# Kernel optimization log

Hardware: AMD Instinct MI355X
Metric: run time of the kernel (lower is better)

## Reference

```python
import jax, jax.numpy as jnp
import numpy as np

N = 50000          # nodes
E = 800000         # edges (before self loops)
D_IN = 128         # input_dim
HID = 64           # hidden_dim (per head)
HEADS = 2
DM = HID * HEADS   # 128, post-concat dim
OUT = 32           # out_channels
G = 64             # graphs in batch
EPS = 1e-5
SLOPE = 0.2        # GATConv negative_slope default


def setup_inputs() -> dict:
    key = jax.random.key(0)
    ks = jax.random.split(key, 24)
    s = 0.1
    return {
        "x": jax.random.normal(ks[0], (N, D_IN), jnp.float32),
        "edge_index": jax.random.randint(ks[1], (2, E), 0, N, jnp.int32),
        "batch": jnp.sort(jax.random.randint(ks[2], (N,), 0, G, jnp.int32)),
        # GAT layer 1
        "W1": jax.random.normal(ks[3], (D_IN, DM), jnp.float32) * s,
        "att_src1": jax.random.normal(ks[4], (HEADS, HID), jnp.float32) * s,
        "att_dst1": jax.random.normal(ks[5], (HEADS, HID), jnp.float32) * s,
        "b1": jnp.zeros((DM,), jnp.float32),
        "ln1_g": jnp.ones((DM,), jnp.float32),
        "ln1_b": jnp.zeros((DM,), jnp.float32),
        # skip connection
        "Wskip": jax.random.normal(ks[6], (D_IN, DM), jnp.float32) * s,
        "bskip": jnp.zeros((DM,), jnp.float32),
        # GAT layer 2
        "W2": jax.random.normal(ks[7], (DM, DM), jnp.float32) * s,
        "att_src2": jax.random.normal(ks[8], (HEADS, HID), jnp.float32) * s,
        "att_dst2": jax.random.normal(ks[9], (HEADS, HID), jnp.float32) * s,
        "b2": jnp.zeros((DM,), jnp.float32),
        "ln2_g": jnp.ones((DM,), jnp.float32),
        "ln2_b": jnp.zeros((DM,), jnp.float32),
        # head
        "Wfc": jax.random.normal(ks[10], (DM, OUT), jnp.float32) * s,
        "bfc": jnp.zeros((OUT,), jnp.float32),
        "bn_g": jnp.ones((OUT,), jnp.float32),
        "bn_b": jnp.zeros((OUT,), jnp.float32),
    }


def _layer_norm(x, g, b):
    m = x.mean(-1, keepdims=True)
    v = ((x - m) ** 2).mean(-1, keepdims=True)
    return (x - m) * jax.lax.rsqrt(v + EPS) * g + b


def _gat(h_in, W, att_src, att_dst, bias, src, dst):
    # PyG GATConv (concat=True): h = x W reshaped to [N,H,C]
    h = (h_in @ W).reshape(N, HEADS, HID)
    a_src = (h * att_src).sum(-1)   # [N,H]
    a_dst = (h * att_dst).sum(-1)   # [N,H]
    e = jax.nn.leaky_relu(a_src[src] + a_dst[dst], SLOPE)  # [E',H]
    # segment softmax over edges sharing target node
    e = e - jax.ops.segment_max(e, dst, num_segments=N)[dst]
    ee = jnp.exp(e)
    denom = jax.ops.segment_sum(ee, dst, num_segments=N)[dst]
    alpha = ee / denom
    msg = h[src] * alpha[:, :, None]               # [E',H,C]
    out = jax.ops.segment_sum(msg, dst, num_segments=N)  # [N,H,C]
    return out.reshape(N, DM) + bias


def reference(x, edge_index, batch, W1, att_src1, att_dst1, b1, ln1_g, ln1_b,
              Wskip, bskip, W2, att_src2, att_dst2, b2, ln2_g, ln2_b,
              Wfc, bfc, bn_g, bn_b):
    # add self loops (PyG GATConv default)
    loop = jnp.arange(N, dtype=edge_index.dtype)
    src = jnp.concatenate([edge_index[0], loop])
    dst = jnp.concatenate([edge_index[1], loop])

    x1 = _gat(x, W1, att_src1, att_dst1, b1, src, dst)
    x1 = jax.nn.elu(_layer_norm(x1, ln1_g, ln1_b))
    x1 = x1 + (x @ Wskip + bskip)          # dropout = identity (eval)

    x2 = _gat(x1, W2, att_src2, att_dst2, b2, src, dst)
    x2 = _layer_norm(x2 + x1, ln2_g, ln2_b)
    emb = jax.nn.elu(x2)

    # global mean pool per graph
    sums = jax.ops.segment_sum(emb, batch, num_segments=G)
    cnt = jax.ops.segment_sum(jnp.ones((N,), emb.dtype), batch, num_segments=G)
    graph_emb = sums / jnp.maximum(cnt, 1.0)[:, None]

    logits = graph_emb @ Wfc + bfc
    # BatchNorm1d (training-mode batch stats, biased var)
    m = logits.mean(0)
    v = ((logits - m) ** 2).mean(0)
    return (logits - m) * jax.lax.rsqrt(v + EPS) * bn_g + bn_b
```

## Files before the change

kernel.cpp:

```cpp
#include <hip/hip_runtime.h>

#define DM    128
#define NHEAD 2
#define HIDC  64
#define OUTC  32
#define NG    64
#define EPS   1e-5f
#define DCAP  64

typedef __attribute__((ext_vector_type(8))) short bf16x8;
typedef __attribute__((ext_vector_type(4))) float f32x4;

__device__ __forceinline__ unsigned short f2bf(float f) {
    union { float f; unsigned int u; } v; v.f = f;
    unsigned int r = v.u + 0x7fffu + ((v.u >> 16) & 1u);
    return (unsigned short)(r >> 16);
}
__device__ __forceinline__ float bflo(unsigned int u) {
    union { unsigned int u; float f; } v; v.u = u << 16; return v.f;
}
__device__ __forceinline__ float bfhi(unsigned int u) {
    union { unsigned int u; float f; } v; v.u = u & 0xffff0000u; return v.f;
}

__global__ void wprep_kernel(const float* __restrict__ W,
                             unsigned short* __restrict__ Wfrag)
{
    const int idx = blockIdx.x * blockDim.x + threadIdx.x;
    if (idx >= 8 * 4 * 64) return;
    const int nt   = idx >> 8;
    const int ks   = (idx >> 6) & 3;
    const int lane = idx & 63;
    const int c    = nt * 16 + (lane & 15);
    const int k0   = ks * 32 + (lane >> 4) * 8;
    bf16x8 f;
#pragma unroll
    for (int j = 0; j < 8; ++j)
        f[j] = (short)f2bf(W[(k0 + j) * DM + c]);
    ((bf16x8*)Wfrag)[idx] = f;
}

__global__ void xprep_kernel(const float* __restrict__ X,
                             unsigned short* __restrict__ Xb, int total)
{
    const int i = (blockIdx.x * blockDim.x + threadIdx.x) * 4;
    if (i >= total) return;
    const float4 v = *(const float4*)&X[i];
    ushort4 o;
    o.x = f2bf(v.x); o.y = f2bf(v.y); o.z = f2bf(v.z); o.w = f2bf(v.w);
    *(ushort4*)&Xb[i] = o;
}

__global__ __launch_bounds__(256) void mfma_gemm_kernel(
    const unsigned short* __restrict__ Xbf, int N,
    const unsigned short* __restrict__ Wfrag,
    const float* __restrict__ bias,
    const float* __restrict__ att_src,
    const float* __restrict__ att_dst,
    float* __restrict__ C,
    unsigned short* __restrict__ Cbf,
    float* __restrict__ a_src,
    float* __restrict__ a_dst)
{
    const int lane = threadIdx.x & 63;
    const int wave = threadIdx.x >> 6;
    const int col  = lane & 15;
    const int kgrp = lane >> 4;

    bf16x8 bfrag[8][4];
    {
        const bf16x8* wf = (const bf16x8*)Wfrag;
#pragma unroll
        for (int nt = 0; nt < 8; ++nt)
#pragma unroll
            for (int ks = 0; ks < 4; ++ks)
                bfrag[nt][ks] = wf[(nt * 4 + ks) * 64 + lane];
    }

    float bcol[8];
#pragma unroll
    for (int nt = 0; nt < 8; ++nt)
        bcol[nt] = bias ? bias[nt * 16 + col] : 0.f;

    float as_c[8], ad_c[8];
    if (att_src) {
#pragma unroll
        for (int nt = 0; nt < 8; ++nt) {
            as_c[nt] = att_src[nt * 16 + col];
            ad_c[nt] = att_dst[nt * 16 + col];
        }
    }

    const int ntiles = (N + 15) >> 4;
    for (int tile = blockIdx.x * 4 + wave; tile < ntiles; tile += gridDim.x * 4) {
        const int row0 = tile * 16;

        f32x4 acc[8];
#pragma unroll
        for (int nt = 0; nt < 8; ++nt) acc[nt] = (f32x4){0.f, 0.f, 0.f, 0.f};

        const int r = min(row0 + col, N - 1);
#pragma unroll
        for (int ks = 0; ks < 4; ++ks) {
            const int k0 = ks * 32 + kgrp * 8;
            const bf16x8 af = *(const bf16x8*)&Xbf[(size_t)r * DM + k0];
#pragma unroll
            for (int nt = 0; nt < 8; ++nt)
                acc[nt] = __builtin_amdgcn_mfma_f32_16x16x32_bf16(
                              af, bfrag[nt][ks], acc[nt], 0, 0, 0);
        }

        float dots[4][2], dotd[4][2];
        if (att_src) {
#pragma unroll
            for (int reg = 0; reg < 4; ++reg) {
                dots[reg][0] = dots[reg][1] = 0.f;
                dotd[reg][0] = dotd[reg][1] = 0.f;
            }
        }
#pragma unroll
        for (int reg = 0; reg < 4; ++reg) {
            const int row = row0 + kgrp * 4 + reg;
            const bool ok = row < N;
#pragma unroll
            for (int nt = 0; nt < 8; ++nt) {
                const float o = acc[nt][reg] + bcol[nt];
                if (ok) {
                    if (Cbf) Cbf[(size_t)row * DM + nt * 16 + col] = f2bf(o);
                    else     C  [(size_t)row * DM + nt * 16 + col] = o;
                }
                if (att_src) {
                    dots[reg][nt >> 2] += o * as_c[nt];
                    dotd[reg][nt >> 2] += o * ad_c[nt];
                }
            }
        }
        if (att_src) {
#pragma unroll
            for (int reg = 0; reg < 4; ++reg) {
#pragma unroll
                for (int h = 0; h < 2; ++h) {
                    float vs = dots[reg][h], vd = dotd[reg][h];
#pragma unroll
                    for (int off = 8; off; off >>= 1) {
                        vs += __shfl_xor(vs, off);
                        vd += __shfl_xor(vd, off);
                    }
                    const int row = row0 + kgrp * 4 + reg;
                    if (col == 0 && row < N) {
                        a_src[row * NHEAD + h] = vs;
                        a_dst[row * NHEAD + h] = vd;
                    }
                }
            }
        }
    }
}

__global__ void scatter_kernel(const int* __restrict__ ei, int E,
                               int* __restrict__ cursor,
                               unsigned short* __restrict__ col)
{
    int e = blockIdx.x * blockDim.x + threadIdx.x;
    if (e < E) {
        int d = ei[E + e];
        int k = atomicAdd(&cursor[d], 1);
        if (k < DCAP) col[d * DCAP + k] = (unsigned short)ei[e];
    }
}

__global__ __launch_bounds__(128) void gat_agg_ln_kernel(
    const int* __restrict__ deg,
    const unsigned short* __restrict__ col,
    const unsigned short* __restrict__ H,
    const float* __restrict__ a_src,
    const float* __restrict__ a_dst,
    const float* __restrict__ bias,
    const float* __restrict__ res,
    const float* __restrict__ lng,
    const float* __restrict__ lnb,
    const float* __restrict__ skip,
    float* __restrict__ out,
    unsigned short* __restrict__ obf,
    int N)
{
    const int wid  = threadIdx.x >> 6;
    const int d    = blockIdx.x * 2 + wid;
    if (d >= N) return;
    const int lane = threadIdx.x & 63;
    const int half = lane >> 5;
    const int c2   = lane * 2;

    const float ad_h = a_dst[d * NHEAD + half];

    float e0 = a_src[d * NHEAD + half] + ad_h;
    e0 = e0 > 0.f ? e0 : 0.2f * e0;
    const float wself = __expf(e0);
    float den = wself;
    float2 acc;
    {
        const unsigned int hu = *(const unsigned int*)&H[(size_t)d * DM + c2];
        acc.x = wself * bflo(hu);
        acc.y = wself * bfhi(hu);
    }

    const int dg = min(deg[d], DCAP);
    const int p0 = d * DCAP;
    for (int base = 0; base < dg; base += 32) {
        const int m = min(32, dg - base);
        const int el = lane & 31;

        float we = 0.f;
        int s = 0;
        if (el < m) {
            s = (int)col[p0 + base + el];
            float a = a_src[s * NHEAD + half] + ad_h;
            a = a > 0.f ? a : 0.2f * a;
            we = __expf(a);
        }
        float ws = we;
#pragma unroll
        for (int off = 1; off < 32; off <<= 1) ws += __shfl_xor(ws, off);
        den += ws;

        const int hsel = lane & 32;
        int e = 0;
        for (; e + 8 <= m; e += 8) {
            int   sv[8];
            float wv[8];
            unsigned int uv[8];
#pragma unroll
            for (int j = 0; j < 8; ++j) {
                sv[j] = __shfl(s, e + j);
                wv[j] = __shfl(we, hsel | (e + j));
            }
#pragma unroll
            for (int j = 0; j < 8; ++j)
                uv[j] = *(const unsigned int*)&H[(size_t)sv[j] * DM + c2];
#pragma unroll
            for (int j = 0; j < 8; ++j) {
                acc.x += wv[j] * bflo(uv[j]);
                acc.y += wv[j] * bfhi(uv[j]);
            }
        }
        for (; e < m; ++e) {
            const int sE = __shfl(s, e);
            const float wE = __shfl(we, hsel | e);
            const unsigned int uE = *(const unsigned int*)&H[(size_t)sE * DM + c2];
            acc.x += wE * bflo(uE);
            acc.y += wE * bfhi(uE);
        }
    }

    const size_t ibase = (size_t)d * DM + c2;
    const float2 bv = *(const float2*)&bias[c2];
    float vx = acc.x / den + bv.x;
    float vy = acc.y / den + bv.y;
    if (res) {
        const float2 r = *(const float2*)&res[ibase];
        vx += r.x; vy += r.y;
    }

    float sm = vx + vy;
#pragma unroll
    for (int off = 1; off < 64; off <<= 1) sm += __shfl_xor(sm, off);
    const float mean = sm * (1.f / DM);

    const float dx = vx - mean, dy = vy - mean;
    float s2 = dx * dx + dy * dy;
#pragma unroll
    for (int off = 1; off < 64; off <<= 1) s2 += __shfl_xor(s2, off);
    const float rstd = rsqrtf(s2 * (1.f / DM) + EPS);

    const float2 gv = *(const float2*)&lng[c2];
    const float2 bb = *(const float2*)&lnb[c2];
    float yx = dx * rstd * gv.x + bb.x;
    float yy = dy * rstd * gv.y + bb.y;
    yx = yx > 0.f ? yx : expm1f(yx);
    yy = yy > 0.f ? yy : expm1f(yy);
    if (skip) {
        const float2 sk = *(const float2*)&skip[ibase];
        yx += sk.x; yy += sk.y;
    }
    *(float2*)&out[ibase] = make_float2(yx, yy);
    if (obf) {
        const unsigned int pk = (unsigned int)f2bf(yx) |
                                ((unsigned int)f2bf(yy) << 16);
        *(unsigned int*)&obf[ibase] = pk;
    }
}

__global__ void pool_kernel(const float* __restrict__ emb,
                            const int* __restrict__ batch, int N,
                            float* __restrict__ sums,
                            float* __restrict__ cnt)
{
    const int t = threadIdx.x;
    const int chunk = (N + gridDim.x - 1) / gridDim.x;
    const int n0 = blockIdx.x * chunk;
    const int n1 = min(N, n0 + chunk);
    if (n0 >= n1) return;

    int cur = batch[n0];
    float acc = 0.f;
    int count = 0;
    for (int n = n0; n < n1; ++n) {
        int b = batch[n];
        if (b != cur) {
            atomicAdd(&sums[cur * DM + t], acc);
            if (t == 0) atomicAdd(&cnt[cur], (float)count);
            acc = 0.f; count = 0; cur = b;
        }
        acc += emb[n * DM + t];
        ++count;
    }
    atomicAdd(&sums[cur * DM + t], acc);
    if (t == 0) atomicAdd(&cnt[cur], (float)count);
}

__global__ void head_kernel(const float* __restrict__ sums,
                            const float* __restrict__ cnt,
                            const float* __restrict__ Wfc,
                            const float* __restrict__ bfc,
                            const float* __restrict__ bn_g,
                            const float* __restrict__ bn_b,
                            float* __restrict__ out)
{
    __shared__ float ge[NG * DM];
    __shared__ float lg[NG * OUTC];
    __shared__ float mu[OUTC], inv[OUTC];
    const int t = threadIdx.x;

    for (int i = t; i < NG * DM; i += blockDim.x) {
        int g = i >> 7;
        ge[i] = sums[i] / fmaxf(cnt[g], 1.0f);
    }
    __syncthreads();

    for (int i = t; i < NG * OUTC; i += blockDim.x) {
        int g = i >> 5, o = i & (OUTC - 1);
        float acc = bfc[o];
#pragma unroll
        for (int k = 0; k < DM; ++k) acc += ge[g * DM + k] * Wfc[k * OUTC + o];
        lg[i] = acc;
    }
    __syncthreads();

    if (t < OUTC) {
        float s = 0.f;
        for (int g = 0; g < NG; ++g) s += lg[g * OUTC + t];
        float m = s * (1.f / NG);
        float v = 0.f;
        for (int g = 0; g < NG; ++g) { float d = lg[g * OUTC + t] - m; v += d * d; }
        v *= (1.f / NG);
        mu[t] = m;
        inv[t] = rsqrtf(v + EPS) * bn_g[t];
    }
    __syncthreads();

    for (int i = t; i < NG * OUTC; i += blockDim.x) {
        int o = i & (OUTC - 1);
        out[i] = (lg[i] - mu[o]) * inv[o] + bn_b[o];
    }
}

extern "C" void kernel_launch(void* const* d_in, const int* in_sizes, int n_in,
                              void* d_out, int out_size, void* d_ws, size_t ws_size,
                              hipStream_t stream)
{
    const float* x     = (const float*)d_in[0];
    const int*   ei    = (const int*)  d_in[1];
    const int*   batch = (const int*)  d_in[2];
    const float* W1    = (const float*)d_in[3];
    const float* as1   = (const float*)d_in[4];
    const float* ad1   = (const float*)d_in[5];
    const float* b1    = (const float*)d_in[6];
    const float* ln1g  = (const float*)d_in[7];
    const float* ln1b  = (const float*)d_in[8];
    const float* Wskip = (const float*)d_in[9];
    const float* bskip = (const float*)d_in[10];
    const float* W2    = (const float*)d_in[11];
    const float* as2   = (const float*)d_in[12];
    const float* ad2   = (const float*)d_in[13];
    const float* b2    = (const float*)d_in[14];
    const float* ln2g  = (const float*)d_in[15];
    const float* ln2b  = (const float*)d_in[16];
    const float* Wfc   = (const float*)d_in[17];
    const float* bfc   = (const float*)d_in[18];
    const float* bng   = (const float*)d_in[19];
    const float* bnb   = (const float*)d_in[20];

    const int N  = in_sizes[2];
    const int E  = in_sizes[1] / 2;

    size_t off = 0;
    auto alloc = [&](size_t bytes) -> char* {
        char* p = (char*)d_ws + off;
        off += (bytes + 255) & ~(size_t)255;
        return p;
    };
    unsigned short* Hbuf   = (unsigned short*)alloc((size_t)N * DM * 2);
    unsigned short* xbf    = (unsigned short*)alloc((size_t)N * DM * 2);
    unsigned short* Buf1bf = (unsigned short*)alloc((size_t)N * DM * 2);
    float* Buf1   = (float*)alloc((size_t)N * DM * 4);
    float* Buf2   = (float*)alloc((size_t)N * DM * 4);
    float* asrc   = (float*)alloc((size_t)N * NHEAD * 4);
    float* adst   = (float*)alloc((size_t)N * NHEAD * 4);
    int*   cursor = (int*)  alloc((size_t)N * 4);
    unsigned short* col = (unsigned short*)alloc((size_t)N * DCAP * 2);
    unsigned short* wf1 = (unsigned short*)alloc((size_t)2048 * 8 * 2);
    unsigned short* wfs = (unsigned short*)alloc((size_t)2048 * 8 * 2);
    unsigned short* wf2 = (unsigned short*)alloc((size_t)2048 * 8 * 2);
    float* sums   = (float*)alloc((size_t)(NG * DM + NG) * 4);
    float* cnt    = sums + NG * DM;

    const int eb = (E + 255) / 256;
    const int ab = (N + 1) / 2;
    const int xb = (N * DM / 4 + 255) / 256;

    hipMemsetAsync(cursor, 0, (size_t)N * 4, stream);
    scatter_kernel<<<eb, 256, 0, stream>>>(ei, E, cursor, col);

    wprep_kernel<<<8, 256, 0, stream>>>(W1, wf1);
    wprep_kernel<<<8, 256, 0, stream>>>(Wskip, wfs);
    wprep_kernel<<<8, 256, 0, stream>>>(W2, wf2);
    xprep_kernel<<<xb, 256, 0, stream>>>(x, xbf, N * DM);

    mfma_gemm_kernel<<<256, 256, 0, stream>>>(xbf, N, wf1, nullptr, as1, ad1,
                                              nullptr, Hbuf, asrc, adst);
    mfma_gemm_kernel<<<256, 256, 0, stream>>>(xbf, N, wfs, bskip, nullptr, nullptr,
                                              Buf2, nullptr, nullptr, nullptr);
    gat_agg_ln_kernel<<<ab, 128, 0, stream>>>(cursor, col, Hbuf, asrc, adst,
                                              b1, nullptr, ln1g, ln1b, Buf2,
                                              Buf1, Buf1bf, N);

    mfma_gemm_kernel<<<256, 256, 0, stream>>>(Buf1bf, N, wf2, nullptr, as2, ad2,
                                              nullptr, Hbuf, asrc, adst);
    gat_agg_ln_kernel<<<ab, 128, 0, stream>>>(cursor, col, Hbuf, asrc, adst,
                                              b2, Buf1, ln2g, ln2b, nullptr,
                                              Buf2, nullptr, N);

    hipMemsetAsync(sums, 0, (size_t)(NG * DM + NG) * 4, stream);
    pool_kernel<<<1024, DM, 0, stream>>>(Buf2, batch, N, sums, cnt);
    head_kernel<<<1, 1024, 0, stream>>>(sums, cnt, Wfc, bfc, bng, bnb, (float*)d_out);
}
```

Before: 248.0 us.

## Fuse prep kernels, pair layer-1 GEMMs, and store intermediates in bf16

Merges edge scatter, weight fragment prep and x conversion into one launch, and runs the W1 and skip GEMMs in a single 512-block launch. Layer outputs are now written only as bf16, so the residual and the pooling step read half the bytes and the fp32 copies are gone. The aggregation inner loop also drops from 8-wide to 4-wide unrolling. Together these cut launch overhead and memory traffic, at the cost of some precision loss in the residual and pooled embeddings.

```diff
diff --git a/kernel.cpp b/kernel.cpp
--- a/kernel.cpp
+++ b/kernel.cpp
@@ -23,35 +23,50 @@
     union { unsigned int u; float f; } v; v.u = u & 0xffff0000u; return v.f;
 }
 
-__global__ void wprep_kernel(const float* __restrict__ W,
-                             unsigned short* __restrict__ Wfrag)
-{
-    const int idx = blockIdx.x * blockDim.x + threadIdx.x;
-    if (idx >= 8 * 4 * 64) return;
-    const int nt   = idx >> 8;
-    const int ks   = (idx >> 6) & 3;
-    const int lane = idx & 63;
-    const int c    = nt * 16 + (lane & 15);
-    const int k0   = ks * 32 + (lane >> 4) * 8;
-    bf16x8 f;
-#pragma unroll
-    for (int j = 0; j < 8; ++j)
-        f[j] = (short)f2bf(W[(k0 + j) * DM + c]);
-    ((bf16x8*)Wfrag)[idx] = f;
-}
-
-__global__ void xprep_kernel(const float* __restrict__ X,
-                             unsigned short* __restrict__ Xb, int total)
-{
-    const int i = (blockIdx.x * blockDim.x + threadIdx.x) * 4;
-    if (i >= total) return;
-    const float4 v = *(const float4*)&X[i];
-    ushort4 o;
-    o.x = f2bf(v.x); o.y = f2bf(v.y); o.z = f2bf(v.z); o.w = f2bf(v.w);
-    *(ushort4*)&Xb[i] = o;
-}
-
-__global__ __launch_bounds__(256) void mfma_gemm_kernel(
+__global__ __launch_bounds__(256) void build_prep_kernel(
+    const int* __restrict__ ei, int E, int eb,
+    int* __restrict__ cursor, unsigned short* __restrict__ col,
+    const float* __restrict__ W1, const float* __restrict__ Wskip,
+    const float* __restrict__ W2,
+    unsigned short* __restrict__ wf1, unsigned short* __restrict__ wfs,
+    unsigned short* __restrict__ wf2,
+    const float* __restrict__ x, unsigned short* __restrict__ xbf, int total)
+{
+    const int b = blockIdx.x;
+    if (b < eb) {
+        const int e = b * 256 + threadIdx.x;
+        if (e < E) {
+            const int d = ei[E + e];
+            const int k = atomicAdd(&cursor[d], 1);
+            if (k < DCAP) col[d * DCAP + k] = (unsigned short)ei[e];
+        }
+    } else if (b < eb + 24) {
+        const int wb = b - eb;
+        const float* W = wb < 8 ? W1 : (wb < 16 ? Wskip : W2);
+        unsigned short* WF = wb < 8 ? wf1 : (wb < 16 ? wfs : wf2);
+        const int idx = (wb & 7) * 256 + threadIdx.x;
+        const int nt   = idx >> 8;
+        const int ks   = (idx >> 6) & 3;
+        const int lane = idx & 63;
+        const int c    = nt * 16 + (lane & 15);
+        const int k0   = ks * 32 + (lane >> 4) * 8;
+        bf16x8 f;
+#pragma unroll
+        for (int j = 0; j < 8; ++j)
+            f[j] = (short)f2bf(W[(k0 + j) * DM + c]);
+        ((bf16x8*)WF)[idx] = f;
+    } else {
+        const int i = ((b - eb - 24) * 256 + threadIdx.x) * 4;
+        if (i < total) {
+            const float4 v = *(const float4*)&x[i];
+            ushort4 o;
+            o.x = f2bf(v.x); o.y = f2bf(v.y); o.z = f2bf(v.z); o.w = f2bf(v.w);
+            *(ushort4*)&xbf[i] = o;
+        }
+    }
+}
+
+__device__ __forceinline__ void gemm_body(
     const unsigned short* __restrict__ Xbf, int N,
     const unsigned short* __restrict__ Wfrag,
     const float* __restrict__ bias,
@@ -60,7 +75,8 @@
     float* __restrict__ C,
     unsigned short* __restrict__ Cbf,
     float* __restrict__ a_src,
-    float* __restrict__ a_dst)
+    float* __restrict__ a_dst,
+    int bid, int nblocks)
 {
     const int lane = threadIdx.x & 63;
     const int wave = threadIdx.x >> 6;
@@ -92,7 +108,7 @@
     }
 
     const int ntiles = (N + 15) >> 4;
-    for (int tile = blockIdx.x * 4 + wave; tile < ntiles; tile += gridDim.x * 4) {
+    for (int tile = bid * 4 + wave; tile < ntiles; tile += nblocks * 4) {
         const int row0 = tile * 16;
 
         f32x4 acc[8];
@@ -157,16 +173,34 @@
     }
 }
 
-__global__ void scatter_kernel(const int* __restrict__ ei, int E,
-                               int* __restrict__ cursor,
-                               unsigned short* __restrict__ col)
-{
-    int e = blockIdx.x * blockDim.x + threadIdx.x;
-    if (e < E) {
-        int d = ei[E + e];
-        int k = atomicAdd(&cursor[d], 1);
-        if (k < DCAP) col[d * DCAP + k] = (unsigned short)ei[e];
-    }
+__global__ __launch_bounds__(256) void gemm_pair_kernel(
+    const unsigned short* __restrict__ Xbf, int N,
+    const unsigned short* __restrict__ wf1,
+    const unsigned short* __restrict__ wfs,
+    const float* __restrict__ bskip,
+    const float* __restrict__ as1, const float* __restrict__ ad1,
+    unsigned short* __restrict__ Hbuf, float* __restrict__ Skip,
+    float* __restrict__ a_src, float* __restrict__ a_dst)
+{
+    if (blockIdx.x < 256)
+        gemm_body(Xbf, N, wf1, nullptr, as1, ad1, nullptr, Hbuf,
+                  a_src, a_dst, blockIdx.x, 256);
+    else
+        gemm_body(Xbf, N, wfs, bskip, nullptr, nullptr, Skip, nullptr,
+                  nullptr, nullptr, blockIdx.x - 256, 256);
+}
+
+__global__ __launch_bounds__(256) void mfma_gemm_kernel(
+    const unsigned short* __restrict__ Xbf, int N,
+    const unsigned short* __restrict__ Wfrag,
+    const float* __restrict__ att_src,
+    const float* __restrict__ att_dst,
+    unsigned short* __restrict__ Cbf,
+    float* __restrict__ a_src,
+    float* __restrict__ a_dst)
+{
+    gemm_body(Xbf, N, Wfrag, nullptr, att_src, att_dst, nullptr, Cbf,
+              a_src, a_dst, blockIdx.x, gridDim.x);
 }
 
 __global__ __launch_bounds__(128) void gat_agg_ln_kernel(
@@ -176,11 +210,10 @@
     const float* __restrict__ a_src,
     const float* __restrict__ a_dst,
     const float* __restrict__ bias,
-    const float* __restrict__ res,
+    const unsigned short* __restrict__ res,
     const float* __restrict__ lng,
     const float* __restrict__ lnb,
     const float* __restrict__ skip,
-    float* __restrict__ out,
     unsigned short* __restrict__ obf,
     int N)
 {
@@ -225,23 +258,17 @@
 
         const int hsel = lane & 32;
         int e = 0;
-        for (; e + 8 <= m; e += 8) {
-            int   sv[8];
-            float wv[8];
-            unsigned int uv[8];
-#pragma unroll
-            for (int j = 0; j < 8; ++j) {
-                sv[j] = __shfl(s, e + j);
-                wv[j] = __shfl(we, hsel | (e + j));
-            }
-#pragma unroll
-            for (int j = 0; j < 8; ++j)
-                uv[j] = *(const unsigned int*)&H[(size_t)sv[j] * DM + c2];
-#pragma unroll
-            for (int j = 0; j < 8; ++j) {
-                acc.x += wv[j] * bflo(uv[j]);
-                acc.y += wv[j] * bfhi(uv[j]);
-            }
+        for (; e + 4 <= m; e += 4) {
+            const int s0 = __shfl(s, e),     s1 = __shfl(s, e + 1);
+            const int s2 = __shfl(s, e + 2), s3 = __shfl(s, e + 3);
+            const float w0 = __shfl(we, hsel | e),       w1 = __shfl(we, hsel | (e + 1));
+            const float w2 = __shfl(we, hsel | (e + 2)), w3 = __shfl(we, hsel | (e + 3));
+            const unsigned int u0 = *(const unsigned int*)&H[(size_t)s0 * DM + c2];
+            const unsigned int u1 = *(const unsigned int*)&H[(size_t)s1 * DM + c2];
+            const unsigned int u2 = *(const unsigned int*)&H[(size_t)s2 * DM + c2];
+            const unsigned int u3 = *(const unsigned int*)&H[(size_t)s3 * DM + c2];
+            acc.x += w0 * bflo(u0) + w1 * bflo(u1) + w2 * bflo(u2) + w3 * bflo(u3);
+            acc.y += w0 * bfhi(u0) + w1 * bfhi(u1) + w2 * bfhi(u2) + w3 * bfhi(u3);
         }
         for (; e < m; ++e) {
             const int sE = __shfl(s, e);
@@ -257,8 +284,8 @@
     float vx = acc.x / den + bv.x;
     float vy = acc.y / den + bv.y;
     if (res) {
-        const float2 r = *(const float2*)&res[ibase];
-        vx += r.x; vy += r.y;
+        const unsigned int ru = *(const unsigned int*)&res[ibase];
+        vx += bflo(ru); vy += bfhi(ru);
     }
 
     float sm = vx + vy;
@@ -282,15 +309,12 @@
         const float2 sk = *(const float2*)&skip[ibase];
         yx += sk.x; yy += sk.y;
     }
-    *(float2*)&out[ibase] = make_float2(yx, yy);
-    if (obf) {
-        const unsigned int pk = (unsigned int)f2bf(yx) |
-                                ((unsigned int)f2bf(yy) << 16);
-        *(unsigned int*)&obf[ibase] = pk;
-    }
-}
-
-__global__ void pool_kernel(const float* __restrict__ emb,
+    const unsigned int pk = (unsigned int)f2bf(yx) |
+                            ((unsigned int)f2bf(yy) << 16);
+    *(unsigned int*)&obf[ibase] = pk;
+}
+
+__global__ void pool_kernel(const unsigned short* __restrict__ emb,
                             const int* __restrict__ batch, int N,
                             float* __restrict__ sums,
                             float* __restrict__ cnt)
@@ -311,7 +335,9 @@
             if (t == 0) atomicAdd(&cnt[cur], (float)count);
             acc = 0.f; count = 0; cur = b;
         }
-        acc += emb[n * DM + t];
+        unsigned short h = emb[(size_t)n * DM + t];
+        union { unsigned int u; float f; } v; v.u = ((unsigned int)h) << 16;
+        acc += v.f;
         ++count;
     }
     atomicAdd(&sums[cur * DM + t], acc);
@@ -402,8 +428,8 @@
     unsigned short* Hbuf   = (unsigned short*)alloc((size_t)N * DM * 2);
     unsigned short* xbf    = (unsigned short*)alloc((size_t)N * DM * 2);
     unsigned short* Buf1bf = (unsigned short*)alloc((size_t)N * DM * 2);
-    float* Buf1   = (float*)alloc((size_t)N * DM * 4);
-    float* Buf2   = (float*)alloc((size_t)N * DM * 4);
+    unsigned short* Buf2bf = (unsigned short*)alloc((size_t)N * DM * 2);
+    float* Skip   = (float*)alloc((size_t)N * DM * 4);
     float* asrc   = (float*)alloc((size_t)N * NHEAD * 4);
     float* adst   = (float*)alloc((size_t)N * NHEAD * 4);
     int*   cursor = (int*)  alloc((size_t)N * 4);
@@ -419,28 +445,23 @@
     const int xb = (N * DM / 4 + 255) / 256;
 
     hipMemsetAsync(cursor, 0, (size_t)N * 4, stream);
-    scatter_kernel<<<eb, 256, 0, stream>>>(ei, E, cursor, col);
-
-    wprep_kernel<<<8, 256, 0, stream>>>(W1, wf1);
-    wprep_kernel<<<8, 256, 0, stream>>>(Wskip, wfs);
-    wprep_kernel<<<8, 256, 0, stream>>>(W2, wf2);
-    xprep_kernel<<<xb, 256, 0, stream>>>(x, xbf, N * DM);
-
-    mfma_gemm_kernel<<<256, 256, 0, stream>>>(xbf, N, wf1, nullptr, as1, ad1,
-                                              nullptr, Hbuf, asrc, adst);
-    mfma_gemm_kernel<<<256, 256, 0, stream>>>(xbf, N, wfs, bskip, nullptr, nullptr,
-                                              Buf2, nullptr, nullptr, nullptr);
+    build_prep_kernel<<<eb + 24 + xb, 256, 0, stream>>>(
+        ei, E, eb, cursor, col, W1, Wskip, W2, wf1, wfs, wf2,
+        x, xbf, N * DM);
+
+    gemm_pair_kernel<<<512, 256, 0, stream>>>(xbf, N, wf1, wfs, bskip,
+                                              as1, ad1, Hbuf, Skip, asrc, adst);
     gat_agg_ln_kernel<<<ab, 128, 0, stream>>>(cursor, col, Hbuf, asrc, adst,
-                                              b1, nullptr, ln1g, ln1b, Buf2,
-                                              Buf1, Buf1bf, N);
-
-    mfma_gemm_kernel<<<256, 256, 0, stream>>>(Buf1bf, N, wf2, nullptr, as2, ad2,
-                                              nullptr, Hbuf, asrc, adst);
+                                              b1, nullptr, ln1g, ln1b, Skip,
+                                              Buf1bf, N);
+
+    mfma_gemm_kernel<<<256, 256, 0, stream>>>(Buf1bf, N, wf2, as2, ad2,
+                                              Hbuf, asrc, adst);
     gat_agg_ln_kernel<<<ab, 128, 0, stream>>>(cursor, col, Hbuf, asrc, adst,
-                                              b2, Buf1, ln2g, ln2b, nullptr,
-                                              Buf2, nullptr, N);
+                                              b2, Buf1bf, ln2g, ln2b, nullptr,
+                                              Buf2bf, N);
 
     hipMemsetAsync(sums, 0, (size_t)(NG * DM + NG) * 4, stream);
-    pool_kernel<<<1024, DM, 0, stream>>>(Buf2, batch, N, sums, cnt);
+    pool_kernel<<<1024, DM, 0, stream>>>(Buf2bf, batch, N, sums, cnt);
     head_kernel<<<1, 1024, 0, stream>>>(sums, cnt, Wfc, bfc, bng, bnb, (float*)d_out);
 }
```

Measured after the change: 226.7 us (median of 2 runs). 1.09x faster.
